# Kernel tuning notes

Measured on AMD Instinct MI355X. Metric: run time of the kernel, lower is better.

The kernel has to match this reference:

```python
import jax, jax.numpy as jnp
import numpy as np

D_MODEL = 256
N_BINS = 11
# standard KNRM kernels: exact-match bin (mu=1, sigma=1e-3) + 10 soft bins
MUS = jnp.array([1.0, 0.9, 0.7, 0.5, 0.3, 0.1, -0.1, -0.3, -0.5, -0.7, -0.9], dtype=jnp.float32)
SIGMAS = jnp.array([1e-3] + [0.1] * 10, dtype=jnp.float32)


def _l2norm(x, eps=1e-10):
    # F.normalize(p=2, eps=1e-10): x / max(||x||, eps)
    n = jnp.sqrt(jnp.sum(x * x, axis=-1, keepdims=True))
    return x / jnp.maximum(n, eps)


def setup_inputs() -> dict:
    key = jax.random.key(0)
    ks = jax.random.split(key, 10)
    B, NB, Q, T, D = 64, 8, 32, 256, D_MODEL
    return {
        "word_atten": jax.random.uniform(ks[0], (B, NB, Q), dtype=jnp.float32),
        "hq": jax.random.normal(ks[1], (B, NB, Q, D), dtype=jnp.float32),
        "can": jax.random.normal(ks[2], (B, T, D), dtype=jnp.float32),
        "rep": jax.random.normal(ks[3], (B, NB, D), dtype=jnp.float32),
        "rep_cur": jax.random.normal(ks[4], (B, D), dtype=jnp.float32),
        "mask_hq": jnp.ones((B, NB, Q), dtype=jnp.float32),
        "mask_can": jnp.ones((B, T), dtype=jnp.float32),
        "mask_session": jnp.ones((B, NB), dtype=jnp.float32),
        "W_dense": jax.random.normal(ks[5], (N_BINS, 1), dtype=jnp.float32) * 0.3,
        "b_dense": jnp.zeros((1,), dtype=jnp.float32),
        "W_att": jax.random.normal(ks[6], (D, D), dtype=jnp.float32) * (1.0 / np.sqrt(D)),
        "b_att": jnp.zeros((D,), dtype=jnp.float32),
    }


def reference(word_atten, hq, can, rep, rep_cur, mask_hq, mask_can, mask_session,
              W_dense, b_dense, W_att, b_att):
    # cosine-similarity matrix: [B, NB, Q, T]
    hq_n = _l2norm(hq)
    can_n = _l2norm(can)
    matrix = jnp.einsum("bnqd,btd->bnqt", hq_n, can_n)

    # Gaussian kernel soft-binning: expand to [B, NB, Q, T, N_BINS]
    diff = matrix[..., None] - MUS  # broadcast over bins
    kern = jnp.exp(-(diff * diff) / (2.0 * SIGMAS * SIGMAS))
    kern = kern * mask_can[:, None, None, :, None]  # mask doc tokens
    pooling_sum = jnp.sum(kern, axis=3)  # [B, NB, Q, N_BINS]

    log_pool = jnp.log(jnp.clip(pooling_sum, 1e-10)) * 0.01
    log_pool = log_pool * mask_hq[..., None] * word_atten[..., None]
    pooled = jnp.sum(log_pool, axis=2)  # [B, NB, N_BINS]

    pooled = pooled * mask_session[..., None]

    # attention over session blocks (AttendAttention): scaled dot with projected current rep
    q = rep_cur @ W_att + b_att  # [B, D]
    scores = jnp.einsum("bnd,bd->bn", rep, q) / np.sqrt(D_MODEL).astype(np.float32)
    scores = jnp.where(mask_session > 0, scores, -1e9)
    attn = jax.nn.softmax(scores, axis=-1)  # [B, NB]

    score = jnp.tanh(pooled @ W_dense + b_dense).squeeze(-1)  # [B, NB]
    return jnp.sum(score * attn, axis=1)  # [B]
```

## Files before the change

### kernel.cpp

```cpp
#include <hip/hip_runtime.h>

#define B_ 64
#define NB_ 8
#define Q_ 32
#define T_ 256
#define D_ 256
#define NBINS 11

typedef __attribute__((ext_vector_type(8))) short bf16x8;
typedef __attribute__((ext_vector_type(4))) float f32x4;
typedef unsigned short ushort_t;
typedef unsigned int uint_t;

__device__ inline ushort_t bf16_rnd(float f) {
  uint_t u = __float_as_uint(f);
  return (ushort_t)((u + 0x8000u) >> 16);
}
__device__ inline uint_t pack2(ushort_t a, ushort_t b) {
  return (uint_t)a | ((uint_t)b << 16);
}

__global__ __launch_bounds__(256) void pool_kernel(
    const float* __restrict__ hq, const float* __restrict__ can,
    const float* __restrict__ word_atten, const float* __restrict__ mask_hq,
    const float* __restrict__ mask_can, float* __restrict__ pooled) {
  __shared__ __align__(16) ushort_t can_hi[32 * 264];
  __shared__ __align__(16) ushort_t can_lo[32 * 264];
  float* partial = (float*)can_hi;
  float* lp_sm = ((float*)can_hi) + 704;

  const float mus[NBINS] = {1.0f, 0.9f, 0.7f, 0.5f, 0.3f, 0.1f,
                            -0.1f, -0.3f, -0.5f, -0.7f, -0.9f};
  const float is2[NBINS] = {5.0e5f, 50.f, 50.f, 50.f, 50.f, 50.f,
                            50.f, 50.f, 50.f, 50.f, 50.f};

  int b = blockIdx.x & 63;
  int nb = blockIdx.x >> 6;
  int outb = b * NB_ + nb;
  int tid = threadIdx.x;
  int wv = tid >> 6, lane = tid & 63;
  int lq = lane & 15, lk = lane >> 4;
  int mtile = wv >> 1, ntile = wv & 1;

  const float* hq_base = hq + (size_t)outb * (Q_ * D_);
  const float* can_base = can + (size_t)b * (T_ * D_);
  const float* maskcan_b = mask_can + b * T_;

  const float* arow = hq_base + (size_t)(mtile * 16 + lq) * D_;
  float sumsq = 0.f;
#pragma unroll
  for (int kk = 0; kk < 8; kk++) {
    const float* p = arow + kk * 32 + lk * 8;
    float4 x = reinterpret_cast<const float4*>(p)[0];
    float4 y = reinterpret_cast<const float4*>(p)[1];
    sumsq += x.x * x.x + x.y * x.y + x.z * x.z + x.w * x.w +
             y.x * y.x + y.y * y.y + y.z * y.z + y.w * y.w;
  }
  sumsq += __shfl_xor(sumsq, 16);
  sumsq += __shfl_xor(sumsq, 32);
  float ainv = 1.0f / fmaxf(sqrtf(sumsq), 1e-10f);

  bf16x8 a_hi[8], a_lo[8];
#pragma unroll
  for (int kk = 0; kk < 8; kk++) {
    const float* p = arow + kk * 32 + lk * 8;
    float4 x = reinterpret_cast<const float4*>(p)[0];
    float4 y = reinterpret_cast<const float4*>(p)[1];
    float v[8] = {x.x, x.y, x.z, x.w, y.x, y.y, y.z, y.w};
    union { bf16x8 v8; ushort_t u[8]; } H, L;
#pragma unroll
    for (int j = 0; j < 8; j++) {
      float s = v[j] * ainv;
      ushort_t h = bf16_rnd(s);
      float hf = __uint_as_float(((uint_t)h) << 16);
      H.u[j] = h;
      L.u[j] = bf16_rnd(s - hf);
    }
    a_hi[kk] = H.v8;
    a_lo[kk] = L.v8;
  }

  float binacc[4][NBINS];
#pragma unroll
  for (int r = 0; r < 4; r++)
#pragma unroll
    for (int j = 0; j < NBINS; j++) binacc[r][j] = 0.0f;

  for (int ch = 0; ch < 8; ch++) {
    __syncthreads();
#pragma unroll
    for (int it = 0; it < 4; it++) {
      int flat = it * 2048 + tid * 8;
      int row = flat >> 8, col = flat & 255;
      int trow = ch * 32 + row;
      const float* src = can_base + (size_t)trow * D_ + col;
      float4 x = reinterpret_cast<const float4*>(src)[0];
      float4 y = reinterpret_cast<const float4*>(src)[1];
      float s = x.x * x.x + x.y * x.y + x.z * x.z + x.w * x.w +
                y.x * y.x + y.y * y.y + y.z * y.z + y.w * y.w;
      s += __shfl_xor(s, 1);
      s += __shfl_xor(s, 2);
      s += __shfl_xor(s, 4);
      s += __shfl_xor(s, 8);
      s += __shfl_xor(s, 16);
      float inv = 1.0f / fmaxf(sqrtf(s), 1e-10f);
      float v[8] = {x.x, x.y, x.z, x.w, y.x, y.y, y.z, y.w};
      ushort_t h[8], l[8];
#pragma unroll
      for (int j = 0; j < 8; j++) {
        float sv = v[j] * inv;
        h[j] = bf16_rnd(sv);
        float hf = __uint_as_float(((uint_t)h[j]) << 16);
        l[j] = bf16_rnd(sv - hf);
      }
      uint4 ph = {pack2(h[0], h[1]), pack2(h[2], h[3]),
                  pack2(h[4], h[5]), pack2(h[6], h[7])};
      uint4 pl = {pack2(l[0], l[1]), pack2(l[2], l[3]),
                  pack2(l[4], l[5]), pack2(l[6], l[7])};
      *reinterpret_cast<uint4*>(&can_hi[row * 264 + col]) = ph;
      *reinterpret_cast<uint4*>(&can_lo[row * 264 + col]) = pl;
    }
    __syncthreads();

    f32x4 acc = {0.f, 0.f, 0.f, 0.f};
    const ushort_t* Bhi = &can_hi[(ntile * 16 + lq) * 264];
    const ushort_t* Blo = &can_lo[(ntile * 16 + lq) * 264];
#pragma unroll
    for (int kk = 0; kk < 8; kk++) {
      int off = kk * 32 + lk * 8;
      bf16x8 bh = *reinterpret_cast<const bf16x8*>(Bhi + off);
      bf16x8 bl = *reinterpret_cast<const bf16x8*>(Blo + off);
      acc = __builtin_amdgcn_mfma_f32_16x16x32_bf16(a_hi[kk], bh, acc, 0, 0, 0);
      acc = __builtin_amdgcn_mfma_f32_16x16x32_bf16(a_lo[kk], bh, acc, 0, 0, 0);
      acc = __builtin_amdgcn_mfma_f32_16x16x32_bf16(a_hi[kk], bl, acc, 0, 0, 0);
    }

    int t0 = ch * 32 + ntile * 16 + lq;
    float mk = maskcan_b[t0];
#pragma unroll
    for (int r = 0; r < 4; r++) {
      float v0 = acc[r];
#pragma unroll
      for (int j = 0; j < NBINS; j++) {
        float d0 = v0 - mus[j];
        binacc[r][j] += mk * __expf(-d0 * d0 * is2[j]);
      }
    }
  }

  __syncthreads();

#pragma unroll
  for (int r = 0; r < 4; r++)
#pragma unroll
    for (int j = 0; j < NBINS; j++) {
      float v = binacc[r][j];
      v += __shfl_xor(v, 1);
      v += __shfl_xor(v, 2);
      v += __shfl_xor(v, 4);
      v += __shfl_xor(v, 8);
      binacc[r][j] = v;
    }
  if (lq == 0) {
#pragma unroll
    for (int r = 0; r < 4; r++)
#pragma unroll
      for (int j = 0; j < NBINS; j++)
        partial[(wv * 16 + lk * 4 + r) * NBINS + j] = binacc[r][j];
  }
  __syncthreads();

  for (int idx = tid; idx < Q_ * NBINS; idx += 256) {
    int q = idx / NBINS;
    int j = idx - q * NBINS;
    int mt = q >> 4, lr = q & 15;
    float sum = partial[((2 * mt) * 16 + lr) * NBINS + j] +
                partial[((2 * mt + 1) * 16 + lr) * NBINS + j];
    float wa = word_atten[outb * Q_ + q] * mask_hq[outb * Q_ + q];
    lp_sm[q * NBINS + j] = logf(fmaxf(sum, 1e-10f)) * 0.01f * wa;
  }
  __syncthreads();

  if (tid < NBINS) {
    float acc2 = 0.f;
#pragma unroll
    for (int q = 0; q < Q_; q++) acc2 += lp_sm[q * NBINS + tid];
    pooled[outb * NBINS + tid] = acc2;
  }
}

__global__ __launch_bounds__(256) void final_kernel(
    const float* __restrict__ rep, const float* __restrict__ rep_cur,
    const float* __restrict__ mask_session, const float* __restrict__ W_dense,
    const float* __restrict__ b_dense, const float* __restrict__ W_att,
    const float* __restrict__ b_att, const float* __restrict__ pooled,
    float* __restrict__ out) {
  __shared__ float qproj[D_];
  __shared__ float scores_sm[NB_];
  int b = blockIdx.x, tid = threadIdx.x;

  const float* rc = rep_cur + b * D_;
  float acc = b_att[tid];
  for (int k = 0; k < D_; k++) acc += rc[k] * W_att[k * D_ + tid];
  qproj[tid] = acc;
  __syncthreads();

  int wv = tid >> 6, lane = tid & 63;
  for (int nn = wv; nn < NB_; nn += 4) {
    const float* rp = rep + ((size_t)b * NB_ + nn) * D_;
    float4 r4 = reinterpret_cast<const float4*>(rp)[lane];
    float4 q4 = *reinterpret_cast<float4*>(&qproj[lane * 4]);
    float s = r4.x * q4.x + r4.y * q4.y + r4.z * q4.z + r4.w * q4.w;
#pragma unroll
    for (int off = 32; off > 0; off >>= 1) s += __shfl_down(s, off);
    if (lane == 0) scores_sm[nn] = s * 0.0625f;
  }
  __syncthreads();

  if (tid == 0) {
    float sc[NB_];
    float mx = -1e30f;
    for (int nn = 0; nn < NB_; nn++) {
      float s = (mask_session[b * NB_ + nn] > 0.f) ? scores_sm[nn] : -1e9f;
      sc[nn] = s;
      mx = fmaxf(mx, s);
    }
    float den = 0.f;
    for (int nn = 0; nn < NB_; nn++) {
      sc[nn] = __expf(sc[nn] - mx);
      den += sc[nn];
    }
    float res = 0.f;
    for (int nn = 0; nn < NB_; nn++) {
      float ms = mask_session[b * NB_ + nn];
      float pw = b_dense[0];
      for (int j = 0; j < NBINS; j++)
        pw += pooled[(b * NB_ + nn) * NBINS + j] * ms * W_dense[j];
      res += tanhf(pw) * (sc[nn] / den);
    }
    out[b] = res;
  }
}

extern "C" void kernel_launch(void* const* d_in, const int* in_sizes, int n_in,
                              void* d_out, int out_size, void* d_ws,
                              size_t ws_size, hipStream_t stream) {
  const float* word_atten = (const float*)d_in[0];
  const float* hq = (const float*)d_in[1];
  const float* can = (const float*)d_in[2];
  const float* rep = (const float*)d_in[3];
  const float* rep_cur = (const float*)d_in[4];
  const float* mask_hq = (const float*)d_in[5];
  const float* mask_can = (const float*)d_in[6];
  const float* mask_session = (const float*)d_in[7];
  const float* W_dense = (const float*)d_in[8];
  const float* b_dense = (const float*)d_in[9];
  const float* W_att = (const float*)d_in[10];
  const float* b_att = (const float*)d_in[11];
  float* out = (float*)d_out;

  float* pooled = (float*)d_ws;

  hipLaunchKernelGGL(pool_kernel, dim3(B_ * NB_), dim3(256), 0, stream, hq, can,
                     word_atten, mask_hq, mask_can, pooled);
  hipLaunchKernelGGL(final_kernel, dim3(B_), dim3(256), 0, stream, rep, rep_cur,
                     mask_session, W_dense, b_dense, W_att, b_att, pooled, out);
}
```

Baseline: 147.9 us.

## Pre-split normalized inputs into MFMA-ready bf16 tiles and split pooling over T

Adds a split kernel that normalizes can and hq once, splits them into bf16 hi/lo pairs and writes them to workspace in MFMA fragment order. Each candidate row was previously renormalized by every (b,nb) block. The pool kernel now runs on 2048 blocks, each taking a quarter of T, loading fragments straight from global memory and accumulating bin sums with atomics. The log/weighting step moves into the final kernel. This costs a memset, an extra launch, workspace traffic and atomics, and it falls back to the old kernels when the workspace is too small.

Result: slower. 212.1 us (+43.5%).

```diff
diff --git a/kernel.cpp b/kernel.cpp
--- a/kernel.cpp
+++ b/kernel.cpp
@@ -12,6 +12,13 @@
 typedef unsigned short ushort_t;
 typedef unsigned int uint_t;
 
+#define CANH_OFF 0u
+#define CANL_OFF 8388608u
+#define HQH_OFF 16777216u
+#define HQL_OFF 25165824u
+#define PSUM_OFF 33554432u
+#define WS_NEED (33554432u + 720896u)
+
 __device__ inline ushort_t bf16_rnd(float f) {
   uint_t u = __float_as_uint(f);
   return (ushort_t)((u + 0x8000u) >> 16);
@@ -20,7 +27,232 @@
   return (uint_t)a | ((uint_t)b << 16);
 }
 
+__global__ __launch_bounds__(256) void split_kernel(
+    const float* __restrict__ can, const float* __restrict__ hq,
+    uint4* __restrict__ canH, uint4* __restrict__ canL,
+    uint4* __restrict__ hqH, uint4* __restrict__ hqL) {
+  __shared__ __align__(16) ushort_t sm_hi[32 * 264];
+  __shared__ __align__(16) ushort_t sm_lo[32 * 264];
+  int blk = blockIdx.x;
+  int tid = threadIdx.x;
+  const float* src;
+  uint4 *dH, *dL;
+  int tilebase;
+  if (blk < 512) {
+    int b = blk >> 3, ch = blk & 7;
+    src = can + ((size_t)b * T_ + ch * 32) * D_;
+    tilebase = b * 16 + ch * 2;
+    dH = canH;
+    dL = canL;
+  } else {
+    int outb = blk - 512;
+    src = hq + (size_t)outb * Q_ * D_;
+    tilebase = outb * 2;
+    dH = hqH;
+    dL = hqL;
+  }
+#pragma unroll
+  for (int it = 0; it < 4; it++) {
+    int flat = it * 2048 + tid * 8;
+    int row = flat >> 8, col = flat & 255;
+    const float* p = src + row * D_ + col;
+    float4 x = reinterpret_cast<const float4*>(p)[0];
+    float4 y = reinterpret_cast<const float4*>(p)[1];
+    float s = x.x * x.x + x.y * x.y + x.z * x.z + x.w * x.w +
+              y.x * y.x + y.y * y.y + y.z * y.z + y.w * y.w;
+    s += __shfl_xor(s, 1);
+    s += __shfl_xor(s, 2);
+    s += __shfl_xor(s, 4);
+    s += __shfl_xor(s, 8);
+    s += __shfl_xor(s, 16);
+    float inv = 1.0f / fmaxf(sqrtf(s), 1e-10f);
+    float v[8] = {x.x, x.y, x.z, x.w, y.x, y.y, y.z, y.w};
+    ushort_t h[8], l[8];
+#pragma unroll
+    for (int j = 0; j < 8; j++) {
+      float sv = v[j] * inv;
+      h[j] = bf16_rnd(sv);
+      float hf = __uint_as_float(((uint_t)h[j]) << 16);
+      l[j] = bf16_rnd(sv - hf);
+    }
+    uint4 ph = {pack2(h[0], h[1]), pack2(h[2], h[3]), pack2(h[4], h[5]),
+                pack2(h[6], h[7])};
+    uint4 pl = {pack2(l[0], l[1]), pack2(l[2], l[3]), pack2(l[4], l[5]),
+                pack2(l[6], l[7])};
+    *reinterpret_cast<uint4*>(&sm_hi[row * 264 + col]) = ph;
+    *reinterpret_cast<uint4*>(&sm_lo[row * 264 + col]) = pl;
+  }
+  __syncthreads();
+  int wv = tid >> 6, lane = tid & 63;
+  int tl = wv >> 1, part = wv & 1;
+  int lq = lane & 15, lk = lane >> 4;
+  const ushort_t* smp = part ? sm_lo : sm_hi;
+  uint4* dst = part ? dL : dH;
+#pragma unroll
+  for (int kk = 0; kk < 8; kk++) {
+    const ushort_t* a = &smp[(tl * 16 + lq) * 264 + kk * 32 + lk * 8];
+    dst[((size_t)(tilebase + tl) * 8 + kk) * 64 + lane] =
+        *reinterpret_cast<const uint4*>(a);
+  }
+}
+
 __global__ __launch_bounds__(256) void pool_kernel(
+    const uint4* __restrict__ canH, const uint4* __restrict__ canL,
+    const uint4* __restrict__ hqH, const uint4* __restrict__ hqL,
+    const float* __restrict__ mask_can, float* __restrict__ psum) {
+  const float mus[NBINS] = {1.0f, 0.9f, 0.7f, 0.5f, 0.3f, 0.1f,
+                            -0.1f, -0.3f, -0.5f, -0.7f, -0.9f};
+  const float nis2[NBINS] = {-5.0e5f, -50.f, -50.f, -50.f, -50.f, -50.f,
+                             -50.f, -50.f, -50.f, -50.f, -50.f};
+  int i = blockIdx.x;
+  int b = i & 63;
+  int nb = (i >> 6) & 7;
+  int tq = i >> 9;
+  int outb = b * NB_ + nb;
+  int tid = threadIdx.x;
+  int wv = tid >> 6, lane = tid & 63;
+  int lq = lane & 15, lk = lane >> 4;
+  int mtile = wv >> 1, th = wv & 1;
+
+  bf16x8 ah[8], al[8];
+  {
+    size_t abase = (size_t)(outb * 2 + mtile) * 8 * 64 + lane;
+#pragma unroll
+    for (int kk = 0; kk < 8; kk++) {
+      ah[kk] = *reinterpret_cast<const bf16x8*>(&hqH[abase + kk * 64]);
+      al[kk] = *reinterpret_cast<const bf16x8*>(&hqL[abase + kk * 64]);
+    }
+  }
+
+  float binacc[4][NBINS];
+#pragma unroll
+  for (int r = 0; r < 4; r++)
+#pragma unroll
+    for (int j = 0; j < NBINS; j++) binacc[r][j] = 0.0f;
+
+#pragma unroll
+  for (int ti = 0; ti < 2; ti++) {
+    int tt = tq * 4 + th * 2 + ti;
+    size_t bbase = (size_t)(b * 16 + tt) * 8 * 64 + lane;
+    f32x4 acc = {0.f, 0.f, 0.f, 0.f};
+#pragma unroll
+    for (int kk = 0; kk < 8; kk++) {
+      bf16x8 bh = *reinterpret_cast<const bf16x8*>(&canH[bbase + kk * 64]);
+      bf16x8 bl = *reinterpret_cast<const bf16x8*>(&canL[bbase + kk * 64]);
+      acc = __builtin_amdgcn_mfma_f32_16x16x32_bf16(ah[kk], bh, acc, 0, 0, 0);
+      acc = __builtin_amdgcn_mfma_f32_16x16x32_bf16(al[kk], bh, acc, 0, 0, 0);
+      acc = __builtin_amdgcn_mfma_f32_16x16x32_bf16(ah[kk], bl, acc, 0, 0, 0);
+    }
+    float mk = mask_can[b * T_ + tt * 16 + lq];
+#pragma unroll
+    for (int r = 0; r < 4; r++) {
+      float v = acc[r];
+#pragma unroll
+      for (int j = 0; j < NBINS; j++) {
+        float d = v - mus[j];
+        binacc[r][j] += mk * __expf(d * d * nis2[j]);
+      }
+    }
+  }
+
+#pragma unroll
+  for (int r = 0; r < 4; r++)
+#pragma unroll
+    for (int j = 0; j < NBINS; j++) {
+      float v = binacc[r][j];
+      v += __shfl_xor(v, 1);
+      v += __shfl_xor(v, 2);
+      v += __shfl_xor(v, 4);
+      v += __shfl_xor(v, 8);
+      binacc[r][j] = v;
+    }
+  if (lq == 0) {
+#pragma unroll
+    for (int r = 0; r < 4; r++) {
+      int q = mtile * 16 + lk * 4 + r;
+#pragma unroll
+      for (int j = 0; j < NBINS; j++)
+        atomicAdd(&psum[(outb * Q_ + q) * NBINS + j], binacc[r][j]);
+    }
+  }
+}
+
+__global__ __launch_bounds__(256) void final_kernel(
+    const float* __restrict__ rep, const float* __restrict__ rep_cur,
+    const float* __restrict__ mask_session, const float* __restrict__ W_dense,
+    const float* __restrict__ b_dense, const float* __restrict__ W_att,
+    const float* __restrict__ b_att, const float* __restrict__ word_atten,
+    const float* __restrict__ mask_hq, const float* __restrict__ psum,
+    float* __restrict__ out) {
+  __shared__ float lp[NB_ * Q_ * NBINS];
+  __shared__ float pooled_sm[NB_ * NBINS];
+  __shared__ float qproj[D_];
+  __shared__ float scores_sm[NB_];
+  int b = blockIdx.x, tid = threadIdx.x;
+
+  {
+    int nb = tid >> 5, q = tid & 31;
+    int outb = b * NB_ + nb;
+    float wa = word_atten[outb * Q_ + q] * mask_hq[outb * Q_ + q];
+    const float* ps = &psum[(outb * Q_ + q) * NBINS];
+#pragma unroll
+    for (int j = 0; j < NBINS; j++)
+      lp[(nb * Q_ + q) * NBINS + j] =
+          logf(fmaxf(ps[j], 1e-10f)) * 0.01f * wa;
+  }
+
+  const float* rc = rep_cur + b * D_;
+  float acc = b_att[tid];
+  for (int k = 0; k < D_; k++) acc += rc[k] * W_att[k * D_ + tid];
+  qproj[tid] = acc;
+  __syncthreads();
+
+  if (tid < NB_ * NBINS) {
+    int nb = tid / NBINS, j = tid - nb * NBINS;
+    float s = 0.f;
+#pragma unroll
+    for (int q = 0; q < Q_; q++) s += lp[(nb * Q_ + q) * NBINS + j];
+    pooled_sm[nb * NBINS + j] = s;
+  }
+
+  int wv = tid >> 6, lane = tid & 63;
+  for (int nn = wv; nn < NB_; nn += 4) {
+    const float* rp = rep + ((size_t)b * NB_ + nn) * D_;
+    float4 r4 = reinterpret_cast<const float4*>(rp)[lane];
+    float4 q4 = *reinterpret_cast<float4*>(&qproj[lane * 4]);
+    float s = r4.x * q4.x + r4.y * q4.y + r4.z * q4.z + r4.w * q4.w;
+#pragma unroll
+    for (int off = 32; off > 0; off >>= 1) s += __shfl_down(s, off);
+    if (lane == 0) scores_sm[nn] = s * 0.0625f;
+  }
+  __syncthreads();
+
+  if (tid == 0) {
+    float sc[NB_];
+    float mx = -1e30f;
+    for (int nn = 0; nn < NB_; nn++) {
+      float s = (mask_session[b * NB_ + nn] > 0.f) ? scores_sm[nn] : -1e9f;
+      sc[nn] = s;
+      mx = fmaxf(mx, s);
+    }
+    float den = 0.f;
+    for (int nn = 0; nn < NB_; nn++) {
+      sc[nn] = __expf(sc[nn] - mx);
+      den += sc[nn];
+    }
+    float res = 0.f;
+    for (int nn = 0; nn < NB_; nn++) {
+      float ms = mask_session[b * NB_ + nn];
+      float pw = b_dense[0];
+      for (int j = 0; j < NBINS; j++)
+        pw += pooled_sm[nn * NBINS + j] * ms * W_dense[j];
+      res += tanhf(pw) * (sc[nn] / den);
+    }
+    out[b] = res;
+  }
+}
+
+__global__ __launch_bounds__(256) void pool_kernel_fb(
     const float* __restrict__ hq, const float* __restrict__ can,
     const float* __restrict__ word_atten, const float* __restrict__ mask_hq,
     const float* __restrict__ mask_can, float* __restrict__ pooled) {
@@ -113,10 +345,10 @@
         float hf = __uint_as_float(((uint_t)h[j]) << 16);
         l[j] = bf16_rnd(sv - hf);
       }
-      uint4 ph = {pack2(h[0], h[1]), pack2(h[2], h[3]),
-                  pack2(h[4], h[5]), pack2(h[6], h[7])};
-      uint4 pl = {pack2(l[0], l[1]), pack2(l[2], l[3]),
-                  pack2(l[4], l[5]), pack2(l[6], l[7])};
+      uint4 ph = {pack2(h[0], h[1]), pack2(h[2], h[3]), pack2(h[4], h[5]),
+                  pack2(h[6], h[7])};
+      uint4 pl = {pack2(l[0], l[1]), pack2(l[2], l[3]), pack2(l[4], l[5]),
+                  pack2(l[6], l[7])};
       *reinterpret_cast<uint4*>(&can_hi[row * 264 + col]) = ph;
       *reinterpret_cast<uint4*>(&can_lo[row * 264 + col]) = pl;
     }
@@ -189,7 +421,7 @@
   }
 }
 
-__global__ __launch_bounds__(256) void final_kernel(
+__global__ __launch_bounds__(256) void final_kernel_fb(
     const float* __restrict__ rep, const float* __restrict__ rep_cur,
     const float* __restrict__ mask_session, const float* __restrict__ W_dense,
     const float* __restrict__ b_dense, const float* __restrict__ W_att,
@@ -259,10 +491,29 @@
   const float* b_att = (const float*)d_in[11];
   float* out = (float*)d_out;
 
-  float* pooled = (float*)d_ws;
-
-  hipLaunchKernelGGL(pool_kernel, dim3(B_ * NB_), dim3(256), 0, stream, hq, can,
-                     word_atten, mask_hq, mask_can, pooled);
-  hipLaunchKernelGGL(final_kernel, dim3(B_), dim3(256), 0, stream, rep, rep_cur,
-                     mask_session, W_dense, b_dense, W_att, b_att, pooled, out);
-}
+  char* ws = (char*)d_ws;
+  if (ws_size >= (size_t)WS_NEED) {
+    uint4* canH = (uint4*)(ws + CANH_OFF);
+    uint4* canL = (uint4*)(ws + CANL_OFF);
+    uint4* hqH = (uint4*)(ws + HQH_OFF);
+    uint4* hqL = (uint4*)(ws + HQL_OFF);
+    float* psum = (float*)(ws + PSUM_OFF);
+
+    hipMemsetAsync(psum, 0, (size_t)B_ * NB_ * Q_ * NBINS * sizeof(float),
+                   stream);
+    hipLaunchKernelGGL(split_kernel, dim3(1024), dim3(256), 0, stream, can, hq,
+                       canH, canL, hqH, hqL);
+    hipLaunchKernelGGL(pool_kernel, dim3(2048), dim3(256), 0, stream, canH,
+                       canL, hqH, hqL, mask_can, psum);
+    hipLaunchKernelGGL(final_kernel, dim3(B_), dim3(256), 0, stream, rep,
+                       rep_cur, mask_session, W_dense, b_dense, W_att, b_att,
+                       word_atten, mask_hq, psum, out);
+  } else {
+    float* pooled = (float*)ws;
+    hipLaunchKernelGGL(pool_kernel_fb, dim3(B_ * NB_), dim3(256), 0, stream,
+                       hq, can, word_atten, mask_hq, mask_can, pooled);
+    hipLaunchKernelGGL(final_kernel_fb, dim3(B_), dim3(256), 0, stream, rep,
+                       rep_cur, mask_session, W_dense, b_dense, W_att, b_att,
+                       pooled, out);
+  }
+}
```

## Split pooling over two T-halves and move log/sum reduction into final kernel

Applied to the files above, without the earlier changes.

The pool kernel grid doubles from 512 to 1024 blocks, with each block handling half of the candidate tokens (128 rows) and writing raw per-query bin sums to a workspace. The final kernel combines the two halves, applies log, word attention and mask, then sums over queries before the dense/attention step. This is meant to raise parallelism and occupancy on the many-CU GPU, where 512 blocks underfill the device. The cost is each block re-normalizing and splitting its hq tile, plus more workspace traffic and extra work in the small final kernel.

Measured after the change: 151.6 us. 1.03x slower.

```diff
diff --git a/kernel.cpp b/kernel.cpp
--- a/kernel.cpp
+++ b/kernel.cpp
@@ -22,20 +22,20 @@
 
 __global__ __launch_bounds__(256) void pool_kernel(
     const float* __restrict__ hq, const float* __restrict__ can,
-    const float* __restrict__ word_atten, const float* __restrict__ mask_hq,
-    const float* __restrict__ mask_can, float* __restrict__ pooled) {
+    const float* __restrict__ mask_can, float* __restrict__ psum) {
   __shared__ __align__(16) ushort_t can_hi[32 * 264];
   __shared__ __align__(16) ushort_t can_lo[32 * 264];
   float* partial = (float*)can_hi;
-  float* lp_sm = ((float*)can_hi) + 704;
 
   const float mus[NBINS] = {1.0f, 0.9f, 0.7f, 0.5f, 0.3f, 0.1f,
                             -0.1f, -0.3f, -0.5f, -0.7f, -0.9f};
-  const float is2[NBINS] = {5.0e5f, 50.f, 50.f, 50.f, 50.f, 50.f,
-                            50.f, 50.f, 50.f, 50.f, 50.f};
-
-  int b = blockIdx.x & 63;
-  int nb = blockIdx.x >> 6;
+  const float nis2[NBINS] = {-5.0e5f, -50.f, -50.f, -50.f, -50.f, -50.f,
+                             -50.f, -50.f, -50.f, -50.f, -50.f};
+
+  int i = blockIdx.x;
+  int b = i & 63;
+  int nb = (i >> 6) & 7;
+  int th = i >> 9;
   int outb = b * NB_ + nb;
   int tid = threadIdx.x;
   int wv = tid >> 6, lane = tid & 63;
@@ -86,13 +86,13 @@
 #pragma unroll
     for (int j = 0; j < NBINS; j++) binacc[r][j] = 0.0f;
 
-  for (int ch = 0; ch < 8; ch++) {
+  for (int ch = 0; ch < 4; ch++) {
     __syncthreads();
 #pragma unroll
     for (int it = 0; it < 4; it++) {
       int flat = it * 2048 + tid * 8;
       int row = flat >> 8, col = flat & 255;
-      int trow = ch * 32 + row;
+      int trow = th * 128 + ch * 32 + row;
       const float* src = can_base + (size_t)trow * D_ + col;
       float4 x = reinterpret_cast<const float4*>(src)[0];
       float4 y = reinterpret_cast<const float4*>(src)[1];
@@ -113,10 +113,10 @@
         float hf = __uint_as_float(((uint_t)h[j]) << 16);
         l[j] = bf16_rnd(sv - hf);
       }
-      uint4 ph = {pack2(h[0], h[1]), pack2(h[2], h[3]),
-                  pack2(h[4], h[5]), pack2(h[6], h[7])};
-      uint4 pl = {pack2(l[0], l[1]), pack2(l[2], l[3]),
-                  pack2(l[4], l[5]), pack2(l[6], l[7])};
+      uint4 ph = {pack2(h[0], h[1]), pack2(h[2], h[3]), pack2(h[4], h[5]),
+                  pack2(h[6], h[7])};
+      uint4 pl = {pack2(l[0], l[1]), pack2(l[2], l[3]), pack2(l[4], l[5]),
+                  pack2(l[6], l[7])};
       *reinterpret_cast<uint4*>(&can_hi[row * 264 + col]) = ph;
       *reinterpret_cast<uint4*>(&can_lo[row * 264 + col]) = pl;
     }
@@ -135,7 +135,7 @@
       acc = __builtin_amdgcn_mfma_f32_16x16x32_bf16(a_hi[kk], bl, acc, 0, 0, 0);
     }
 
-    int t0 = ch * 32 + ntile * 16 + lq;
+    int t0 = th * 128 + ch * 32 + ntile * 16 + lq;
     float mk = maskcan_b[t0];
 #pragma unroll
     for (int r = 0; r < 4; r++) {
@@ -143,7 +143,7 @@
 #pragma unroll
       for (int j = 0; j < NBINS; j++) {
         float d0 = v0 - mus[j];
-        binacc[r][j] += mk * __expf(-d0 * d0 * is2[j]);
+        binacc[r][j] += mk * __expf(d0 * d0 * nis2[j]);
       }
     }
   }
@@ -170,22 +170,13 @@
   }
   __syncthreads();
 
+  float* dst = &psum[(size_t)(outb * 2 + th) * (Q_ * NBINS)];
   for (int idx = tid; idx < Q_ * NBINS; idx += 256) {
     int q = idx / NBINS;
     int j = idx - q * NBINS;
     int mt = q >> 4, lr = q & 15;
-    float sum = partial[((2 * mt) * 16 + lr) * NBINS + j] +
-                partial[((2 * mt + 1) * 16 + lr) * NBINS + j];
-    float wa = word_atten[outb * Q_ + q] * mask_hq[outb * Q_ + q];
-    lp_sm[q * NBINS + j] = logf(fmaxf(sum, 1e-10f)) * 0.01f * wa;
-  }
-  __syncthreads();
-
-  if (tid < NBINS) {
-    float acc2 = 0.f;
-#pragma unroll
-    for (int q = 0; q < Q_; q++) acc2 += lp_sm[q * NBINS + tid];
-    pooled[outb * NBINS + tid] = acc2;
+    dst[idx] = partial[((2 * mt) * 16 + lr) * NBINS + j] +
+               partial[((2 * mt + 1) * 16 + lr) * NBINS + j];
   }
 }
 
@@ -193,17 +184,41 @@
     const float* __restrict__ rep, const float* __restrict__ rep_cur,
     const float* __restrict__ mask_session, const float* __restrict__ W_dense,
     const float* __restrict__ b_dense, const float* __restrict__ W_att,
-    const float* __restrict__ b_att, const float* __restrict__ pooled,
+    const float* __restrict__ b_att, const float* __restrict__ word_atten,
+    const float* __restrict__ mask_hq, const float* __restrict__ psum,
     float* __restrict__ out) {
+  __shared__ float lp[NB_ * Q_ * NBINS];
+  __shared__ float pooled_sm[NB_ * NBINS];
   __shared__ float qproj[D_];
   __shared__ float scores_sm[NB_];
   int b = blockIdx.x, tid = threadIdx.x;
+
+  {
+    int nb = tid >> 5, q = tid & 31;
+    int outb = b * NB_ + nb;
+    float wa = word_atten[outb * Q_ + q] * mask_hq[outb * Q_ + q];
+    const float* p0 = &psum[(size_t)(outb * 2 + 0) * (Q_ * NBINS) + q * NBINS];
+    const float* p1 = &psum[(size_t)(outb * 2 + 1) * (Q_ * NBINS) + q * NBINS];
+#pragma unroll
+    for (int j = 0; j < NBINS; j++) {
+      float s = p0[j] + p1[j];
+      lp[(nb * Q_ + q) * NBINS + j] = logf(fmaxf(s, 1e-10f)) * 0.01f * wa;
+    }
+  }
 
   const float* rc = rep_cur + b * D_;
   float acc = b_att[tid];
   for (int k = 0; k < D_; k++) acc += rc[k] * W_att[k * D_ + tid];
   qproj[tid] = acc;
   __syncthreads();
+
+  if (tid < NB_ * NBINS) {
+    int nb = tid / NBINS, j = tid - nb * NBINS;
+    float s = 0.f;
+#pragma unroll
+    for (int q = 0; q < Q_; q++) s += lp[(nb * Q_ + q) * NBINS + j];
+    pooled_sm[nb * NBINS + j] = s;
+  }
 
   int wv = tid >> 6, lane = tid & 63;
   for (int nn = wv; nn < NB_; nn += 4) {
@@ -235,7 +250,7 @@
       float ms = mask_session[b * NB_ + nn];
       float pw = b_dense[0];
       for (int j = 0; j < NBINS; j++)
-        pw += pooled[(b * NB_ + nn) * NBINS + j] * ms * W_dense[j];
+        pw += pooled_sm[nn * NBINS + j] * ms * W_dense[j];
       res += tanhf(pw) * (sc[nn] / den);
     }
     out[b] = res;
@@ -259,10 +274,11 @@
   const float* b_att = (const float*)d_in[11];
   float* out = (float*)d_out;
 
-  float* pooled = (float*)d_ws;
-
-  hipLaunchKernelGGL(pool_kernel, dim3(B_ * NB_), dim3(256), 0, stream, hq, can,
-                     word_atten, mask_hq, mask_can, pooled);
-  hipLaunchKernelGGL(final_kernel, dim3(B_), dim3(256), 0, stream, rep, rep_cur,
-                     mask_session, W_dense, b_dense, W_att, b_att, pooled, out);
-}
+  float* psum = (float*)d_ws;
+
+  hipLaunchKernelGGL(pool_kernel, dim3(1024), dim3(256), 0, stream, hq, can,
+                     mask_can, psum);
+  hipLaunchKernelGGL(final_kernel, dim3(B_), dim3(256), 0, stream, rep,
+                     rep_cur, mask_session, W_dense, b_dense, W_att, b_att,
+                     word_atten, mask_hq, psum, out);
+}
```
